# Optimization experiments

Hardware: AMD Instinct MI355X
Metric: run time of the kernel (lower is better)

## Reference

```python
import jax, jax.numpy as jnp
import numpy as np

TEMP = 0.07
LAMBDA_NODE = 1.0
LAMBDA_GRAPH = 1.0


def _hungarian(cost):
    """Min-cost assignment (Jonker-Volgenant style potentials Hungarian).
    cost: [n, n] numpy float64. Returns col index assigned to each row (row_ind = arange(n))."""
    n = cost.shape[0]
    u = np.zeros(n + 1)
    v = np.zeros(n + 1)
    p = np.zeros(n + 1, dtype=np.int64)   # p[j] = row matched to column j (1-based, 0 = none)
    way = np.zeros(n + 1, dtype=np.int64)
    for i in range(1, n + 1):
        p[0] = i
        j0 = 0
        minv = np.full(n + 1, np.inf)
        used = np.zeros(n + 1, dtype=bool)
        while True:
            used[j0] = True
            i0 = p[j0]
            cur = cost[i0 - 1] - u[i0] - v[1:]          # reduced costs of row i0, len n
            mask = ~used[1:]
            upd = mask & (cur < minv[1:])
            minv[1:][upd] = cur[upd]
            way[1:][upd] = j0
            cand = np.where(mask, minv[1:], np.inf)
            j1 = int(np.argmin(cand)) + 1
            delta = cand[j1 - 1]
            u[p[used]] += delta
            v[used] -= delta
            minv[~used] -= delta
            j0 = j1
            if p[j0] == 0:
                break
        while j0 != 0:                                   # augment along alternating path
            j1 = way[j0]
            p[j0] = p[j1]
            j0 = j1
    col_for_row = np.zeros(n, dtype=np.int64)
    for j in range(1, n + 1):
        col_for_row[p[j] - 1] = j - 1
    return col_for_row


def _l2norm(x, axis):
    return x / jnp.maximum(jnp.linalg.norm(x, axis=axis, keepdims=True), 1e-12)


def setup_inputs() -> dict:
    key = jax.random.key(0)
    ks = jax.random.split(key, 6)
    B, N, D = 128, 128, 1024
    return {
        "v_g": jax.random.normal(ks[0], (B, D), jnp.float32),
        "t_g": jax.random.normal(ks[1], (B, D), jnp.float32),
        "V": jax.random.normal(ks[2], (B, N, D), jnp.float32),
        "T": jax.random.normal(ks[3], (B, N, D), jnp.float32),
        "A_v": jax.random.uniform(ks[4], (B, N, N), jnp.float32),
        "A_t": jax.random.uniform(ks[5], (B, N, N), jnp.float32),
    }


def reference(v_g, t_g, V, T, A_v, A_t):
    # ---- global InfoNCE ----
    vn = _l2norm(v_g, 1)
    tn = _l2norm(t_g, 1)
    sim = (vn @ tn.T) / TEMP                              # [B, B]
    l_i2t = -jnp.mean(jnp.diagonal(jax.nn.log_softmax(sim, axis=1)))
    l_t2i = -jnp.mean(jnp.diagonal(jax.nn.log_softmax(sim.T, axis=1)))
    L_global = 0.5 * (l_i2t + l_t2i)

    # ---- node alignment via Hungarian matching (indices are non-differentiable) ----
    Vn = _l2norm(V, -1)
    Tn = _l2norm(T, -1)
    cost = 1.0 - jnp.einsum("bnd,bmd->bnm", Vn, Tn)       # [B, N, N]
    cost_np = np.asarray(jax.device_get(cost), dtype=np.float64)
    cols = jnp.asarray(np.stack([_hungarian(cost_np[b]) for b in range(cost_np.shape[0])]))
    aligned_T = jnp.take_along_axis(T, cols[:, :, None], axis=1)   # [B, N, D]
    # per-sample mse then mean over batch == global mean since all samples same size
    L_node = jnp.mean((V - aligned_T) ** 2)

    # ---- graph structure mse ----
    L_graph = jnp.mean((A_v - A_t) ** 2)

    total = L_global + LAMBDA_NODE * L_node + LAMBDA_GRAPH * L_graph
    return (total, L_global, L_node, L_graph)
```

## Files before the change

### kernel.cpp

```cpp
#include <hip/hip_runtime.h>
#include <hip/hip_fp16.h>
#include <math.h>

#define TEMPERATURE 0.07f

#define WS_COST    0
#define WS_SIM     2097152
#define WS_COLS    2113536
#define WS_RNV     2129920
#define WS_RNT     2146304
#define WS_PNODE   2162688
#define WS_PGRAPH  2162816
#define WS_ACC     2162944

typedef __attribute__((ext_vector_type(8))) short short8v;
typedef __attribute__((ext_vector_type(4))) float f32x4;

__device__ __forceinline__ short bf16rne(float f) {
    unsigned int u = __float_as_uint(f);
    u += 0x7FFFu + ((u >> 16) & 1u);
    return (short)(u >> 16);
}
__device__ __forceinline__ short8v cvt8s(const float* __restrict__ p, float& ssq) {
    float4 x = *(const float4*)p;
    float4 y = *(const float4*)(p + 4);
    ssq += x.x * x.x + x.y * x.y + x.z * x.z + x.w * x.w
         + y.x * y.x + y.y * y.y + y.z * y.z + y.w * y.w;
    short8v r;
    r[0] = bf16rne(x.x); r[1] = bf16rne(x.y);
    r[2] = bf16rne(x.z); r[3] = bf16rne(x.w);
    r[4] = bf16rne(y.x); r[5] = bf16rne(y.y);
    r[6] = bf16rne(y.z); r[7] = bf16rne(y.w);
    return r;
}

template<bool COSTMODE>
__device__ __forceinline__ void cos_tile(const float* __restrict__ Vb,
                                         const float* __restrict__ Tb,
                                         int half, int tid,
                                         float* __restrict__ outp,
                                         float* __restrict__ rnV,
                                         float* __restrict__ rnT) {
    int w = tid >> 6;
    int lane = tid & 63;
    int n0 = half * 64 + (w >> 1) * 32;
    int m0 = (w & 1) * 64;
    int ar = lane & 15, kq = lane >> 4;
    float qA0 = 0.0f, qA1 = 0.0f, qB0 = 0.0f, qB1 = 0.0f, qB2 = 0.0f, qB3 = 0.0f;
    f32x4 zero = {0.0f, 0.0f, 0.0f, 0.0f};
    f32x4 acc[2][4];
#pragma unroll
    for (int i = 0; i < 2; i++)
#pragma unroll
        for (int j = 0; j < 4; j++) acc[i][j] = zero;

    for (int k0 = 0; k0 < 1024; k0 += 32) {
        int ko = k0 + kq * 8;
        short8v a0 = cvt8s(&Vb[(size_t)(n0 + ar) * 1024 + ko], qA0);
        short8v a1 = cvt8s(&Vb[(size_t)(n0 + 16 + ar) * 1024 + ko], qA1);
        short8v b0 = cvt8s(&Tb[(size_t)(m0 + ar) * 1024 + ko], qB0);
        short8v b1 = cvt8s(&Tb[(size_t)(m0 + 16 + ar) * 1024 + ko], qB1);
        short8v b2 = cvt8s(&Tb[(size_t)(m0 + 32 + ar) * 1024 + ko], qB2);
        short8v b3 = cvt8s(&Tb[(size_t)(m0 + 48 + ar) * 1024 + ko], qB3);
        acc[0][0] = __builtin_amdgcn_mfma_f32_16x16x32_bf16(a0, b0, acc[0][0], 0, 0, 0);
        acc[0][1] = __builtin_amdgcn_mfma_f32_16x16x32_bf16(a0, b1, acc[0][1], 0, 0, 0);
        acc[0][2] = __builtin_amdgcn_mfma_f32_16x16x32_bf16(a0, b2, acc[0][2], 0, 0, 0);
        acc[0][3] = __builtin_amdgcn_mfma_f32_16x16x32_bf16(a0, b3, acc[0][3], 0, 0, 0);
        acc[1][0] = __builtin_amdgcn_mfma_f32_16x16x32_bf16(a1, b0, acc[1][0], 0, 0, 0);
        acc[1][1] = __builtin_amdgcn_mfma_f32_16x16x32_bf16(a1, b1, acc[1][1], 0, 0, 0);
        acc[1][2] = __builtin_amdgcn_mfma_f32_16x16x32_bf16(a1, b2, acc[1][2], 0, 0, 0);
        acc[1][3] = __builtin_amdgcn_mfma_f32_16x16x32_bf16(a1, b3, acc[1][3], 0, 0, 0);
    }
    qA0 += __shfl_xor(qA0, 16); qA0 += __shfl_xor(qA0, 32);
    qA1 += __shfl_xor(qA1, 16); qA1 += __shfl_xor(qA1, 32);
    qB0 += __shfl_xor(qB0, 16); qB0 += __shfl_xor(qB0, 32);
    qB1 += __shfl_xor(qB1, 16); qB1 += __shfl_xor(qB1, 32);
    qB2 += __shfl_xor(qB2, 16); qB2 += __shfl_xor(qB2, 32);
    qB3 += __shfl_xor(qB3, 16); qB3 += __shfl_xor(qB3, 32);
    if (COSTMODE && kq == 0) {
        rnV[n0 + ar]      = sqrtf(qA0);
        rnV[n0 + 16 + ar] = sqrtf(qA1);
        rnT[m0 + ar]      = sqrtf(qB0);
        rnT[m0 + 16 + ar] = sqrtf(qB1);
        rnT[m0 + 32 + ar] = sqrtf(qB2);
        rnT[m0 + 48 + ar] = sqrtf(qB3);
    }
    float invA0 = 1.0f / fmaxf(sqrtf(qA0), 1e-12f);
    float invA1 = 1.0f / fmaxf(sqrtf(qA1), 1e-12f);
    float invB[4];
    invB[0] = 1.0f / fmaxf(sqrtf(qB0), 1e-12f);
    invB[1] = 1.0f / fmaxf(sqrtf(qB1), 1e-12f);
    invB[2] = 1.0f / fmaxf(sqrtf(qB2), 1e-12f);
    invB[3] = 1.0f / fmaxf(sqrtf(qB3), 1e-12f);
#pragma unroll
    for (int i = 0; i < 2; i++) {
        float ia[4];
#pragma unroll
        for (int r = 0; r < 4; r++)
            ia[r] = __shfl(i ? invA1 : invA0, kq * 4 + r);
#pragma unroll
        for (int j = 0; j < 4; j++)
#pragma unroll
            for (int r = 0; r < 4; r++) {
                int rowi = n0 + i * 16 + kq * 4 + r;
                int colj = m0 + j * 16 + ar;
                float cs = acc[i][j][r] * ia[r] * invB[j];
                outp[(size_t)rowi * 128 + colj] =
                    COSTMODE ? (1.0f - cs) : (cs * (1.0f / TEMPERATURE));
            }
    }
}

__global__ __launch_bounds__(256) void k_cost(const float* __restrict__ V,
                                              const float* __restrict__ T,
                                              float* __restrict__ cost,
                                              float* __restrict__ rnV,
                                              float* __restrict__ rnT) {
    int b = blockIdx.x >> 1;
    int half = blockIdx.x & 1;
    cos_tile<true>(V + (size_t)b * 131072, T + (size_t)b * 131072, half, threadIdx.x,
                   cost + (size_t)b * 16384, rnV + b * 128, rnT + b * 128);
}

#define HUNG_INF 3.0e38f

__device__ __forceinline__ int rdlane_i(int v, int l) {
    return __builtin_amdgcn_readlane(v, l);
}
__device__ __forceinline__ float rdlane_f(float v, int l) {
    return __int_as_float(__builtin_amdgcn_readlane(__float_as_int(v), l));
}

__device__ __forceinline__ unsigned int dpp_umin_wave(unsigned int x) {
    int o;
    o = __builtin_amdgcn_update_dpp(-1, (int)x, 0x111, 0xF, 0xF, false);
    x = (x < (unsigned int)o) ? x : (unsigned int)o;
    o = __builtin_amdgcn_update_dpp(-1, (int)x, 0x112, 0xF, 0xF, false);
    x = (x < (unsigned int)o) ? x : (unsigned int)o;
    o = __builtin_amdgcn_update_dpp(-1, (int)x, 0x114, 0xF, 0xF, false);
    x = (x < (unsigned int)o) ? x : (unsigned int)o;
    o = __builtin_amdgcn_update_dpp(-1, (int)x, 0x118, 0xF, 0xF, false);
    x = (x < (unsigned int)o) ? x : (unsigned int)o;
    o = __builtin_amdgcn_update_dpp(-1, (int)x, 0x142, 0xF, 0xF, false);
    x = (x < (unsigned int)o) ? x : (unsigned int)o;
    o = __builtin_amdgcn_update_dpp(-1, (int)x, 0x143, 0xF, 0xF, false);
    x = (x < (unsigned int)o) ? x : (unsigned int)o;
    return x;
}

template<int CTRL>
__device__ __forceinline__ void dpp2min(unsigned int& a, unsigned int& b) {
    unsigned int ao = (unsigned int)__builtin_amdgcn_update_dpp(-1, (int)a, CTRL, 0xF, 0xF, false);
    unsigned int bo = (unsigned int)__builtin_amdgcn_update_dpp(-1, (int)b, CTRL, 0xF, 0xF, false);
    unsigned int hi = a > ao ? a : ao;
    a = a < ao ? a : ao;
    b = b < bo ? b : bo;
    b = b < hi ? b : hi;
}

__device__ __forceinline__ unsigned int pack_h2(float a, float b) {
    unsigned int ua = (unsigned int)__half_as_ushort(__float2half(a));
    unsigned int ub = (unsigned int)__half_as_ushort(__float2half(b));
    return ua | (ub << 16);
}
__device__ __forceinline__ float h2_lo(unsigned int u) {
    return __half2float(__ushort_as_half((unsigned short)(u & 0xFFFFu)));
}
__device__ __forceinline__ float h2_hi(unsigned int u) {
    return __half2float(__ushort_as_half((unsigned short)(u >> 16)));
}
__device__ __forceinline__ unsigned int vkey(float v, int idx) {
    return (__float_as_uint(v + 1.0f) & 0xFFFFFF80u) | (unsigned int)idx;
}

__global__ __launch_bounds__(256) void k_main(const float* __restrict__ cost,
                                              int* __restrict__ cols,
                                              const float* __restrict__ vg,
                                              const float* __restrict__ tg,
                                              float* __restrict__ sim,
                                              const float* __restrict__ Av,
                                              const float* __restrict__ At,
                                              float* __restrict__ pg) {
    int bid = blockIdx.x;
    int t = threadIdx.x;
    __shared__ unsigned int P[8192];
    __shared__ int freelist[136];
    __shared__ float wsumg[4];

    if (bid >= 130) {
        int idx = bid - 130;
        float s = 0.0f;
        for (int it = 0; it < 16; ++it) {
            size_t off = (((size_t)idx * 16 + it) * 256 + t) * 4;
            float4 a = *(const float4*)&Av[off];
            float4 bb = *(const float4*)&At[off];
            float dx = a.x - bb.x, dy = a.y - bb.y, dz = a.z - bb.z, dw = a.w - bb.w;
            s += dx * dx + dy * dy + dz * dz + dw * dw;
        }
#pragma unroll
        for (int off = 32; off > 0; off >>= 1) s += __shfl_xor(s, off);
        if ((t & 63) == 0) wsumg[t >> 6] = s;
        __syncthreads();
        if (t == 0) pg[idx] = wsumg[0] + wsumg[1] + wsumg[2] + wsumg[3];
        return;
    }
    if (bid >= 128) {
        cos_tile<false>(vg, tg, bid - 128, t, sim, (float*)0, (float*)0);
        return;
    }

    int b = bid;
    const float* C = cost + (size_t)b * 16384;
    for (int i = t; i < 8192; i += 256) {
        int r = i >> 6, l = i & 63;
        P[i] = pack_h2(C[r * 128 + l], C[r * 128 + 64 + l]);
    }
    __syncthreads();
    if (t >= 64) return;
    int lane = t;

    float vA = HUNG_INF, vB = HUNG_INF;
    int yA = 0, yB = 0;
    for (int r = 0; r < 128; ++r) {
        unsigned int pk = P[r * 64 + lane];
        float a = h2_lo(pk), bb = h2_hi(pk);
        if (a < vA) { vA = a; yA = r; }
        if (bb < vB) { vB = bb; yB = r; }
    }
    int p0 = -1, p1 = -1;
    int x0 = -1, x1 = -1;
    float u0 = 0.0f, u1 = 0.0f;
    for (int j = 127; j >= 0; --j) {
        int yi = rdlane_i(j >= 64 ? yB : yA, j & 63);
        int xi = rdlane_i(yi >= 64 ? x1 : x0, yi & 63);
        if (xi < 0) {
            if (lane == (yi & 63)) { if (yi < 64) x0 = j; else x1 = j; }
            if (lane == (j & 63)) { if (j < 64) p0 = yi; else p1 = yi; }
        }
    }

    {
        unsigned int pkc = P[lane];
        for (int i = 0; i < 128; ++i) {
            unsigned int pkn = (i < 127) ? P[(i + 1) * 64 + lane] : 0u;
            int j1 = rdlane_i(i >= 64 ? x1 : x0, i & 63);
            if (j1 >= 0) {
                float rc0 = h2_lo(pkc) - vA;
                float rc1 = h2_hi(pkc) - vB;
                unsigned int k0 = (j1 < 64 && lane == j1) ? 0xFFFFFFFFu : vkey(rc0, lane);
                unsigned int k1 = (j1 >= 64 && lane == (j1 - 64)) ? 0xFFFFFFFFu : vkey(rc1, lane + 64);
                unsigned int km = dpp_umin_wave(k0 < k1 ? k0 : k1);
                unsigned int ka = (unsigned int)rdlane_i((int)km, 63);
                float min2 = __uint_as_float(ka & 0xFFFFFF80u) - 1.0f;
                if (lane == (j1 & 63)) { if (j1 < 64) vA -= min2; else vB -= min2; }
                if (lane == (i & 63)) { if (i < 64) u0 = min2; else u1 = min2; }
            }
            pkc = pkn;
        }
    }

    unsigned long long fm0 = __ballot(x0 < 0);
    unsigned long long fm1 = __ballot(x1 < 0);
    int half0 = __popcll(fm0);
    int nfree = half0 + __popcll(fm1);
    if (x0 < 0) freelist[__popcll(fm0 & ((1ull << lane) - 1))] = lane;
    if (x1 < 0) freelist[half0 + __popcll(fm1 & ((1ull << lane) - 1))] = lane + 64;

    for (int pass = 0; pass < 2 && nfree > 0; ++pass) {
        int cur = 0, nnew = 0, rr = 0;
        while (cur < nfree) {
            int fi = freelist[cur]; cur++;
            rr++;
            if (rr >= 600 || rr >= cur * 128) {
                if (lane == 0) freelist[nnew] = fi;
                nnew++;
                continue;
            }
            unsigned int pk = P[fi * 64 + lane];
            float rc0 = h2_lo(pk) - vA;
            float rc1 = h2_hi(pk) - vB;
            unsigned int k0 = vkey(rc0, lane);
            unsigned int k1 = vkey(rc1, lane + 64);
            unsigned int a = k0 < k1 ? k0 : k1;
            unsigned int bk = k0 < k1 ? k1 : k0;
            dpp2min<0x111>(a, bk); dpp2min<0x112>(a, bk); dpp2min<0x114>(a, bk);
            dpp2min<0x118>(a, bk); dpp2min<0x142>(a, bk); dpp2min<0x143>(a, bk);
            unsigned int ka = (unsigned int)rdlane_i((int)a, 63);
            unsigned int kb = (unsigned int)rdlane_i((int)bk, 63);
            int j1 = (int)(ka & 127u);
            float vmin = __uint_as_float(ka & 0xFFFFFF80u) - 1.0f;
            float vsec = __uint_as_float(kb & 0xFFFFFF80u) - 1.0f;
            bool lowers = (ka & 0xFFFFFF80u) < (kb & 0xFFFFFF80u);
            int i0 = rdlane_i(j1 >= 64 ? p1 : p0, j1 & 63);
            if (lowers) {
                if (lane == (j1 & 63)) {
                    if (j1 < 64) vA -= (vsec - vmin); else vB -= (vsec - vmin);
                }
            } else if (i0 >= 0) {
                j1 = (int)(kb & 127u);
                i0 = rdlane_i(j1 >= 64 ? p1 : p0, j1 & 63);
            }
            if (i0 >= 0) {
                if (lowers) { cur--; if (lane == 0) freelist[cur] = i0; }
                else { if (lane == 0) freelist[nnew] = i0; nnew++; }
            }
            if (lane == (j1 & 63)) { if (j1 < 64) p0 = fi; else p1 = fi; }
            if (lane == (fi & 63)) { if (fi < 64) u0 = vsec; else u1 = vsec; }
        }
        nfree = nnew;
    }

    for (int fx = 0; fx < nfree; ++fx) {
        int row = freelist[fx];
        float minv0 = HUNG_INF, minv1 = HUNG_INF;
        int way0 = 128, way1 = 128;
        bool used0 = false, used1 = false;
        bool intree0 = (row < 64) && (lane == row);
        bool intree1 = (row >= 64) && (lane == row - 64);
        int j0 = 128;
        int i0r = row;
        while (true) {
            float ui = rdlane_f(i0r >= 64 ? u1 : u0, i0r & 63);
            unsigned int pk = P[i0r * 64 + lane];
            float cur0 = h2_lo(pk) - ui - vA;
            float cur1 = h2_hi(pk) - ui - vB;
            if (!used0 && cur0 < minv0) { minv0 = cur0; way0 = j0; }
            if (!used1 && cur1 < minv1) { minv1 = cur1; way1 = j0; }
            float cand0 = used0 ? HUNG_INF : minv0;
            float cand1 = used1 ? HUNG_INF : minv1;
            unsigned int k0 = vkey(cand0, lane);
            unsigned int k1 = vkey(cand1, lane + 64);
            unsigned int km = dpp_umin_wave(k0 < k1 ? k0 : k1);
            unsigned int kmin = (unsigned int)rdlane_i((int)km, 63);
            int j1 = (int)(kmin & 127u);
            float delta = __uint_as_float(kmin & 0xFFFFFF80u) - 1.0f;
            if (used0) vA -= delta; else minv0 -= delta;
            if (used1) vB -= delta; else minv1 -= delta;
            if (intree0) u0 += delta;
            if (intree1) u1 += delta;
            int pj = rdlane_i(j1 >= 64 ? p1 : p0, j1 & 63);
            if (pj >= 0) {
                if (lane == (j1 & 63)) { if (j1 >= 64) used1 = true; else used0 = true; }
                if (lane == (pj & 63)) { if (pj < 64) intree0 = true; else intree1 = true; }
                j0 = j1;
                i0r = pj;
            } else {
                int j = j1;
                while (j != 128) {
                    int w = rdlane_i(j >= 64 ? way1 : way0, j & 63);
                    int pw = (w == 128) ? row : rdlane_i(w >= 64 ? p1 : p0, w & 63);
                    if (lane == (j & 63)) { if (j >= 64) p1 = pw; else p0 = pw; }
                    j = w;
                }
                break;
            }
        }
    }
    cols[b * 128 + p0] = lane;
    cols[b * 128 + p1] = lane + 64;
}

__global__ __launch_bounds__(128) void k_gn(const float* __restrict__ rnV,
                                            const float* __restrict__ rnT,
                                            const float* __restrict__ cost,
                                            const int* __restrict__ cols,
                                            float* __restrict__ pn,
                                            const float* __restrict__ sim,
                                            float* __restrict__ accg) {
    int t = threadIdx.x;
    if (blockIdx.x == 128) {
        __shared__ float S[128 * 128];
        __shared__ float red[128];
        for (int i = t * 4; i < 16384; i += 512)
            *(float4*)&S[i] = *(const float4*)&sim[i];
        __syncthreads();
        float m = -3e38f, m2 = -3e38f;
        for (int j = 0; j < 128; j++) {
            m = fmaxf(m, S[t * 128 + j]);
            m2 = fmaxf(m2, S[j * 128 + t]);
        }
        float s = 0.0f, s2 = 0.0f;
        for (int j = 0; j < 128; j++) {
            s += expf(S[t * 128 + j] - m);
            s2 += expf(S[j * 128 + t] - m2);
        }
        float contrib = 2.0f * S[t * 128 + t] - (m + logf(s)) - (m2 + logf(s2));
        red[t] = contrib;
        __syncthreads();
        for (int o = 64; o > 0; o >>= 1) {
            if (t < o) red[t] += red[t + o];
            __syncthreads();
        }
        if (t == 0) accg[0] = -red[0] / 256.0f;
        return;
    }
    int b = blockIdx.x;
    int c = cols[b * 128 + t];
    float nv = rnV[b * 128 + t];
    float nt = rnT[b * 128 + c];
    float Cv = cost[((size_t)b * 128 + t) * 128 + c];
    float s = nv * nv + nt * nt - 2.0f * nv * nt * (1.0f - Cv);
#pragma unroll
    for (int off = 32; off > 0; off >>= 1) s += __shfl_xor(s, off);
    __shared__ float w2[2];
    if ((t & 63) == 0) w2[t >> 6] = s;
    __syncthreads();
    if (t == 0) pn[b] = w2[0] + w2[1];
}

__global__ __launch_bounds__(128) void k_final(const float* __restrict__ accg,
                                               const float* __restrict__ pn,
                                               const float* __restrict__ pg,
                                               float* __restrict__ out) {
    __shared__ float r1[128], r2[128];
    int t = threadIdx.x;
    r1[t] = pn[t];
    r2[t] = pg[t];
    __syncthreads();
    for (int o = 64; o > 0; o >>= 1) {
        if (t < o) { r1[t] += r1[t + o]; r2[t] += r2[t + o]; }
        __syncthreads();
    }
    if (t == 0) {
        float lg = accg[0];
        float ln = r1[0] / 16777216.0f;
        float lgr = r2[0] / 2097152.0f;
        out[0] = lg + ln + lgr;
        out[1] = lg;
        out[2] = ln;
        out[3] = lgr;
    }
}

extern "C" void kernel_launch(void* const* d_in, const int* in_sizes, int n_in,
                              void* d_out, int out_size, void* d_ws, size_t ws_size,
                              hipStream_t stream) {
    const float* vg = (const float*)d_in[0];
    const float* tg = (const float*)d_in[1];
    const float* V  = (const float*)d_in[2];
    const float* T  = (const float*)d_in[3];
    const float* Av = (const float*)d_in[4];
    const float* At = (const float*)d_in[5];
    float* out = (float*)d_out;
    float* ws = (float*)d_ws;

    float* cost = ws + WS_COST;
    float* sim  = ws + WS_SIM;
    int*   cols = (int*)(ws + WS_COLS);
    float* rnV  = ws + WS_RNV;
    float* rnT  = ws + WS_RNT;
    float* pn   = ws + WS_PNODE;
    float* pg   = ws + WS_PGRAPH;
    float* acc  = ws + WS_ACC;

    k_cost<<<256, 256, 0, stream>>>(V, T, cost, rnV, rnT);
    k_main<<<258, 256, 0, stream>>>(cost, cols, vg, tg, sim, Av, At, pg);
    k_gn<<<129, 128, 0, stream>>>(rnV, rnT, cost, cols, pn, sim, acc);
    k_final<<<1, 128, 0, stream>>>(acc, pn, pg, out);
}
```

Measured before the change: 405.9 us.

## Perturb costs with column-index jitter and extend auction-style augmenting passes

Adds a tiny per-column epsilon to the half-precision costs so ties are broken consistently. The aim is to cut down on ties that stall the reduction-transfer and augmenting-row passes. The free-row pass loop now runs three passes instead of two, drops the rr>=cur*128 cutoff, and carries the displaced row in a register with its cost row prefetched rather than pushing it back onto the shared freelist. The jitter slightly changes the cost matrix, which could alter the chosen matching when near-ties exist.

```diff
diff --git a/kernel.cpp b/kernel.cpp
--- a/kernel.cpp
+++ b/kernel.cpp
@@ -123,6 +123,7 @@
 }
 
 #define HUNG_INF 3.0e38f
+#define JEPS 3.0517578125e-05f
 
 __device__ __forceinline__ int rdlane_i(int v, int l) {
     return __builtin_amdgcn_readlane(v, l);
@@ -163,11 +164,11 @@
     unsigned int ub = (unsigned int)__half_as_ushort(__float2half(b));
     return ua | (ub << 16);
 }
-__device__ __forceinline__ float h2_lo(unsigned int u) {
-    return __half2float(__ushort_as_half((unsigned short)(u & 0xFFFFu)));
-}
-__device__ __forceinline__ float h2_hi(unsigned int u) {
-    return __half2float(__ushort_as_half((unsigned short)(u >> 16)));
+__device__ __forceinline__ float jlo(unsigned int u, int lane) {
+    return __half2float(__ushort_as_half((unsigned short)(u & 0xFFFFu))) + (float)lane * JEPS;
+}
+__device__ __forceinline__ float jhi(unsigned int u, int lane) {
+    return __half2float(__ushort_as_half((unsigned short)(u >> 16))) + (float)(lane + 64) * JEPS;
 }
 __device__ __forceinline__ unsigned int vkey(float v, int idx) {
     return (__float_as_uint(v + 1.0f) & 0xFFFFFF80u) | (unsigned int)idx;
@@ -223,7 +224,7 @@
     int yA = 0, yB = 0;
     for (int r = 0; r < 128; ++r) {
         unsigned int pk = P[r * 64 + lane];
-        float a = h2_lo(pk), bb = h2_hi(pk);
+        float a = jlo(pk, lane), bb = jhi(pk, lane);
         if (a < vA) { vA = a; yA = r; }
         if (bb < vB) { vB = bb; yB = r; }
     }
@@ -245,8 +246,8 @@
             unsigned int pkn = (i < 127) ? P[(i + 1) * 64 + lane] : 0u;
             int j1 = rdlane_i(i >= 64 ? x1 : x0, i & 63);
             if (j1 >= 0) {
-                float rc0 = h2_lo(pkc) - vA;
-                float rc1 = h2_hi(pkc) - vB;
+                float rc0 = jlo(pkc, lane) - vA;
+                float rc1 = jhi(pkc, lane) - vB;
                 unsigned int k0 = (j1 < 64 && lane == j1) ? 0xFFFFFFFFu : vkey(rc0, lane);
                 unsigned int k1 = (j1 >= 64 && lane == (j1 - 64)) ? 0xFFFFFFFFu : vkey(rc1, lane + 64);
                 unsigned int km = dpp_umin_wave(k0 < k1 ? k0 : k1);
@@ -266,19 +267,23 @@
     if (x0 < 0) freelist[__popcll(fm0 & ((1ull << lane) - 1))] = lane;
     if (x1 < 0) freelist[half0 + __popcll(fm1 & ((1ull << lane) - 1))] = lane + 64;
 
-    for (int pass = 0; pass < 2 && nfree > 0; ++pass) {
+    for (int pass = 0; pass < 3 && nfree > 0; ++pass) {
         int cur = 0, nnew = 0, rr = 0;
-        while (cur < nfree) {
-            int fi = freelist[cur]; cur++;
+        int pending = -1;
+        unsigned int pkPre = 0;
+        while (pending >= 0 || cur < nfree) {
+            int fi;
+            unsigned int pk;
+            if (pending >= 0) { fi = pending; pk = pkPre; pending = -1; }
+            else { fi = freelist[cur++]; pk = P[fi * 64 + lane]; }
             rr++;
-            if (rr >= 600 || rr >= cur * 128) {
+            if (rr >= 600) {
                 if (lane == 0) freelist[nnew] = fi;
                 nnew++;
                 continue;
             }
-            unsigned int pk = P[fi * 64 + lane];
-            float rc0 = h2_lo(pk) - vA;
-            float rc1 = h2_hi(pk) - vB;
+            float rc0 = jlo(pk, lane) - vA;
+            float rc1 = jhi(pk, lane) - vB;
             unsigned int k0 = vkey(rc0, lane);
             unsigned int k1 = vkey(rc1, lane + 64);
             unsigned int a = k0 < k1 ? k0 : k1;
@@ -301,8 +306,13 @@
                 i0 = rdlane_i(j1 >= 64 ? p1 : p0, j1 & 63);
             }
             if (i0 >= 0) {
-                if (lowers) { cur--; if (lane == 0) freelist[cur] = i0; }
-                else { if (lane == 0) freelist[nnew] = i0; nnew++; }
+                if (lowers) {
+                    pending = i0;
+                    pkPre = P[i0 * 64 + lane];
+                } else {
+                    if (lane == 0) freelist[nnew] = i0;
+                    nnew++;
+                }
             }
             if (lane == (j1 & 63)) { if (j1 < 64) p0 = fi; else p1 = fi; }
             if (lane == (fi & 63)) { if (fi < 64) u0 = vsec; else u1 = vsec; }
@@ -322,8 +332,8 @@
         while (true) {
             float ui = rdlane_f(i0r >= 64 ? u1 : u0, i0r & 63);
             unsigned int pk = P[i0r * 64 + lane];
-            float cur0 = h2_lo(pk) - ui - vA;
-            float cur1 = h2_hi(pk) - ui - vB;
+            float cur0 = jlo(pk, lane) - ui - vA;
+            float cur1 = jhi(pk, lane) - ui - vB;
             if (!used0 && cur0 < minv0) { minv0 = cur0; way0 = j0; }
             if (!used1 && cur1 < minv1) { minv1 = cur1; way1 = j0; }
             float cand0 = used0 ? HUNG_INF : minv0;
```

Measured after the change: 403.0 us. No clear change (-0.7%).
